# Optimization experiments

Hardware: AMD Instinct MI355X
Metric: run time of the kernel (lower is better)

Reference implementation:

```python
import jax, jax.numpy as jnp
import numpy as np

B, C, G, E, R, T, L, K = 8, 192, 256, 384, 4, 8192, 3, 3
DILATIONS = (1, 3, 9)
EPS = 1e-5


def setup_inputs() -> dict:
    key = jax.random.key(0)
    ks = jax.random.split(key, 16)
    s = 0.05
    return {
        'x': jax.random.normal(ks[0], (B, C, T), jnp.float32),
        'x_mask': jnp.ones((B, 1, T), jnp.float32),
        'g': jax.random.normal(ks[1], (B, G, 1), jnp.float32),
        'dconv_w': jax.random.normal(ks[2], (L, C, K), jnp.float32) * s,
        'dconv_b': jax.random.normal(ks[3], (L, C), jnp.float32) * s,
        'ln_gamma': jnp.ones((L, C), jnp.float32),
        'ln_beta': jnp.zeros((L, C), jnp.float32),
        'p1_w': jax.random.normal(ks[4], (L, E, C), jnp.float32) * s,
        'p1_b': jax.random.normal(ks[5], (L, E), jnp.float32) * s,
        'p1_ain_w': jax.random.normal(ks[6], (L, C * R, G), jnp.float32) * 0.01,
        'p1_ain_b': jnp.zeros((L, C * R), jnp.float32),
        'p1_aout_w': jax.random.normal(ks[7], (L, E * R, G), jnp.float32) * 0.01,
        'p1_aout_b': jnp.zeros((L, E * R), jnp.float32),
        'p2_w': jax.random.normal(ks[8], (L, C, E), jnp.float32) * s,
        'p2_b': jax.random.normal(ks[9], (L, C), jnp.float32) * s,
        'p2_ain_w': jax.random.normal(ks[10], (L, E * R, G), jnp.float32) * 0.01,
        'p2_ain_b': jnp.zeros((L, E * R), jnp.float32),
        'p2_aout_w': jax.random.normal(ks[11], (L, C * R, G), jnp.float32) * 0.01,
        'p2_aout_b': jnp.zeros((L, C * R), jnp.float32),
    }


def _causal_dconv(x, w, b, dilation):
    # x: [B,C,T]; w: [C,K] depthwise kernel; matches flip/pad/conv/flip in torch module
    xf = jnp.flip(x, 2)
    xf = jnp.pad(xf, ((0, 0), (0, 0), (0, (K - 1) * dilation)))
    y = jax.lax.conv_general_dilated(
        xf, w[:, None, :], window_strides=(1,), padding='VALID',
        rhs_dilation=(dilation,), dimension_numbers=('NCH', 'OIH', 'NCH'),
        feature_group_count=C)
    y = y + b[None, :, None]
    return jnp.flip(y, 2)


def _layernorm_c(x, gamma, beta):
    # LayerNorm over channel axis (axis=1)
    mu = jnp.mean(x, axis=1, keepdims=True)
    var = jnp.mean(jnp.square(x - mu), axis=1, keepdims=True)
    xn = (x - mu) * jax.lax.rsqrt(var + EPS)
    return xn * gamma[None, :, None] + beta[None, :, None]


def _lora(x, g2, w_main, b_main, ain_w, ain_b, aout_w, aout_b, cin, cout):
    # main 1x1 conv
    x_ = jnp.einsum('oc,bcl->bol', w_main, x) + b_main[None, :, None]
    a_in = (g2 @ ain_w.T + ain_b).reshape(-1, cin, R)      # [B,cin,R]
    a_out = (g2 @ aout_w.T + aout_b).reshape(-1, R, cout)  # [B,R,cout]
    t = jnp.einsum('bcl,bcr->brl', x, a_in)
    low = jnp.einsum('brl,brc->bcl', t, a_out)
    return x_ + low


def reference(x, x_mask, g, dconv_w, dconv_b, ln_gamma, ln_beta,
              p1_w, p1_b, p1_ain_w, p1_ain_b, p1_aout_w, p1_aout_b,
              p2_w, p2_b, p2_ain_w, p2_ain_b, p2_aout_w, p2_aout_b):
    g2 = g[:, :, 0]  # [B,G]
    x = x * x_mask
    for i in range(L):
        residual = x
        h = _causal_dconv(x, dconv_w[i], dconv_b[i], DILATIONS[i])
        h = _layernorm_c(h, ln_gamma[i], ln_beta[i])
        h = h * x_mask
        h = _lora(h, g2, p1_w[i], p1_b[i], p1_ain_w[i], p1_ain_b[i],
                  p1_aout_w[i], p1_aout_b[i], C, E)
        h = jax.nn.gelu(h, approximate=False)
        h = _lora(h, g2, p2_w[i], p2_b[i], p2_ain_w[i], p2_ain_b[i],
                  p2_aout_w[i], p2_aout_b[i], E, C)
        x = residual + h
    return x
```

## Files before the change

### kernel.cpp

```cpp
#include <hip/hip_runtime.h>
#include <hip/hip_bf16.h>

#define B_ 8
#define C_ 192
#define G_ 256
#define E_ 384
#define R_ 4
#define T_ 8192
#define L_ 3
#define K_ 3

typedef __attribute__((ext_vector_type(4))) float f32x4;
typedef __attribute__((ext_vector_type(8))) short bf16x8;
typedef __attribute__((ext_vector_type(4))) short bf16x4;

static __device__ __forceinline__ float bf2f(short u) {
    union { float f; unsigned int i; } z;
    z.i = ((unsigned int)(unsigned short)u) << 16;
    return z.f;
}

static __device__ __forceinline__ float gelu_fast(float x) {
    float x2 = x * x;
    float inner = fmaf(0.044715f * x, x2, x);
    float e = __expf(1.5957691216057308f * inner);
    float r = 1.0f / (e + 1.0f);
    float t = fmaf(-2.0f, r, 1.0f);
    float s = 0.5f * x;
    return fmaf(s, t, s);
}

__global__ __launch_bounds__(256) void adapters_kernel(
    const float* __restrict__ g2,
    const float* __restrict__ w0, const float* __restrict__ bi0, float* __restrict__ o0,
    const float* __restrict__ w1, const float* __restrict__ bi1, float* __restrict__ o1,
    const float* __restrict__ w2, const float* __restrict__ bi2, float* __restrict__ o2,
    const float* __restrict__ w3, const float* __restrict__ bi3, float* __restrict__ o3)
{
    const int N0 = L_ * B_ * (C_ * R_);
    const int N1 = L_ * B_ * (E_ * R_);
    int idx = blockIdx.x * 256 + threadIdx.x;
    const float* w; const float* bi; float* o; int rows; int li;
    if (idx < N0)                      { w=w0; bi=bi0; o=o0; rows=C_*R_; li=idx; }
    else if ((idx -= N0) < N1)         { w=w1; bi=bi1; o=o1; rows=E_*R_; li=idx; }
    else if ((idx -= N1) < N1)         { w=w2; bi=bi2; o=o2; rows=E_*R_; li=idx; }
    else if ((idx -= N1) < N0)         { w=w3; bi=bi3; o=o3; rows=C_*R_; li=idx; }
    else return;
    int bb = li & 7;
    int lr = li >> 3;
    const float4* wr = (const float4*)(w + (size_t)lr * G_);
    const float4* gb = (const float4*)(g2 + (size_t)bb * G_);
    float s = bi[lr];
#pragma unroll 8
    for (int g = 0; g < G_ / 4; ++g) {
        float4 a = gb[g], b = wr[g];
        s = fmaf(a.x, b.x, s); s = fmaf(a.y, b.y, s);
        s = fmaf(a.z, b.z, s); s = fmaf(a.w, b.w, s);
    }
    o[((size_t)(lr / rows) * B_ + bb) * rows + (lr % rows)] = s;
}

__global__ __launch_bounds__(256) void builds_kernel(
    const float* __restrict__ p1w, const float* __restrict__ p2w,
    const float* __restrict__ A1in, const float* __restrict__ A1out,
    const float* __restrict__ A2in, const float* __restrict__ A2out,
    __hip_bfloat16* __restrict__ W1, __hip_bfloat16* __restrict__ W2)
{
    const int W1B = (L_ * B_ * E_ * C_) / 256;
    int blk = blockIdx.x;
    if (blk < W1B) {
        int idx = blk * 256 + threadIdx.x;
        int c = idx % C_;
        int e = (idx / C_) % E_;
        int b = (idx / (C_ * E_)) % B_;
        int l = idx / (C_ * E_ * B_);
        float v = p1w[((size_t)l * E_ + e) * C_ + c];
        const float* ai = A1in + ((size_t)l * B_ + b) * (C_ * R_);
        const float* ao = A1out + ((size_t)l * B_ + b) * (R_ * E_);
#pragma unroll
        for (int r = 0; r < R_; ++r) v = fmaf(ai[c * R_ + r], ao[r * E_ + e], v);
        W1[idx] = __float2bfloat16(v);
    } else {
        int idx = (blk - W1B) * 256 + threadIdx.x;
        int e = idx % E_;
        int c = (idx / E_) % C_;
        int b = (idx / (C_ * E_)) % B_;
        int l = idx / (C_ * E_ * B_);
        float v = p2w[((size_t)l * C_ + c) * E_ + e];
        const float* ai = A2in + ((size_t)l * B_ + b) * (E_ * R_);
        const float* ao = A2out + ((size_t)l * B_ + b) * (R_ * C_);
#pragma unroll
        for (int r = 0; r < R_; ++r) v = fmaf(ai[e * R_ + r], ao[r * C_ + c], v);
        W2[idx] = __float2bfloat16(v);
    }
}

__global__ __launch_bounds__(256) void transpose_in_kernel(
    const float* __restrict__ x, const float* __restrict__ mask,
    __hip_bfloat16* __restrict__ xw)
{
    __shared__ float tile[64][65];
    int b = blockIdx.z, c0 = blockIdx.y * 64, t0 = blockIdx.x * 64;
#pragma unroll
    for (int it = 0; it < 4; ++it) {
        int i = it * 256 + threadIdx.x;
        int r = i >> 4, cq = i & 15;
        float4 xv = *(const float4*)(&x[((size_t)b * C_ + c0 + r) * T_ + t0 + cq * 4]);
        float4 mv = *(const float4*)(&mask[(size_t)b * T_ + t0 + cq * 4]);
        tile[r][cq * 4 + 0] = xv.x * mv.x;
        tile[r][cq * 4 + 1] = xv.y * mv.y;
        tile[r][cq * 4 + 2] = xv.z * mv.z;
        tile[r][cq * 4 + 3] = xv.w * mv.w;
    }
    __syncthreads();
#pragma unroll
    for (int it = 0; it < 4; ++it) {
        int i = it * 256 + threadIdx.x;
        int r = i >> 4, cq = i & 15;
        union { __hip_bfloat16 h[4]; int2 i2; } u;
#pragma unroll
        for (int j = 0; j < 4; ++j) u.h[j] = __float2bfloat16(tile[cq * 4 + j][r]);
        *(int2*)(&xw[((size_t)b * T_ + t0 + r) * C_ + c0 + cq * 4]) = u.i2;
    }
}

__global__ __launch_bounds__(256, 2) void ffn_fused_kernel(
    const __hip_bfloat16* __restrict__ xin, __hip_bfloat16* __restrict__ xout,
    const float* __restrict__ dw, const float* __restrict__ db,
    const float* __restrict__ gamma, const float* __restrict__ beta,
    const float* __restrict__ mask,
    const __hip_bfloat16* __restrict__ W1, const float* __restrict__ b1,
    const __hip_bfloat16* __restrict__ W2, const float* __restrict__ b2,
    int dil, float* __restrict__ outF)
{
    __shared__ __align__(16) char smem[75776];
    __hip_bfloat16 (*Hs)[C_ + 8]  = (__hip_bfloat16 (*)[C_ + 8])smem;
    __hip_bfloat16 (*H1s)[E_ + 8] = (__hip_bfloat16 (*)[E_ + 8])(smem + 25600);

    const int bid = blockIdx.x;
    const int b = bid & 7;
    const int t0 = (bid >> 3) * 64;
    const int tid = threadIdx.x;
    const int wv = tid >> 6, lane = tid & 63;
    const int llo = lane & 15, lhi = lane >> 4;
    const size_t xbase = (size_t)b * T_ * C_;

    {
        const int grp = tid >> 4, gl = tid & 15;
        const int cbase = gl * 12;
        float4 wf[9], dbf[3], gaf[3], bef[3];
#pragma unroll
        for (int q = 0; q < 9; ++q) wf[q] = *(const float4*)(dw + cbase * 3 + q * 4);
#pragma unroll
        for (int q = 0; q < 3; ++q) {
            dbf[q] = *(const float4*)(db + cbase + q * 4);
            gaf[q] = *(const float4*)(gamma + cbase + q * 4);
            bef[q] = *(const float4*)(beta + cbase + q * 4);
        }
#pragma unroll
        for (int rr = 0; rr < 4; ++rr) {
            int tl = grp * 4 + rr;
            int t = t0 + tl;
            float v[12];
#pragma unroll
            for (int j = 0; j < 12; ++j) v[j] = ((const float*)dbf)[j];
#pragma unroll
            for (int k3 = 0; k3 < 3; ++k3) {
                int tt = t - k3 * dil;
                if (tt >= 0) {
                    const __hip_bfloat16* rp = xin + xbase + (size_t)tt * C_ + cbase;
#pragma unroll
                    for (int q = 0; q < 3; ++q) {
                        bf16x4 xv = *(const bf16x4*)(rp + q * 4);
#pragma unroll
                        for (int jj = 0; jj < 4; ++jj) {
                            int j = q * 4 + jj;
                            v[j] = fmaf(((const float*)wf)[j * 3 + k3], bf2f(xv[jj]), v[j]);
                        }
                    }
                }
            }
            float s = 0.f, sq = 0.f;
#pragma unroll
            for (int j = 0; j < 12; ++j) { s += v[j]; sq = fmaf(v[j], v[j], sq); }
#pragma unroll
            for (int o = 1; o <= 8; o <<= 1) {
                s += __shfl_xor(s, o, 64);
                sq += __shfl_xor(sq, o, 64);
            }
            float mu = s * (1.f / C_);
            float var = fmaf(sq, 1.f / C_, -mu * mu);
            float rs = rsqrtf(var + 1e-5f);
            float m = mask[(size_t)b * T_ + t];
            union { __hip_bfloat16 h[12]; int2 i2[3]; } u;
#pragma unroll
            for (int j = 0; j < 12; ++j) {
                float xn = (v[j] - mu) * rs;
                u.h[j] = __float2bfloat16(
                    fmaf(xn, ((const float*)gaf)[j], ((const float*)bef)[j]) * m);
            }
#pragma unroll
            for (int q = 0; q < 3; ++q)
                *(int2*)(&Hs[tl][cbase + q * 4]) = u.i2[q];
        }
    }
    __syncthreads();

    const __hip_bfloat16* w1p = W1 + (size_t)b * E_ * C_
        + (size_t)(wv * 96 + llo) * C_ + lhi * 8;
    f32x4 acc1[6][4] = {};
#pragma unroll
    for (int kc = 0; kc < 6; ++kc) {
        bf16x8 bfr[4];
#pragma unroll
        for (int nf = 0; nf < 4; ++nf)
            bfr[nf] = *(const bf16x8*)(&Hs[nf * 16 + llo][kc * 32 + lhi * 8]);
#pragma unroll
        for (int mf = 0; mf < 6; ++mf) {
            bf16x8 af = *(const bf16x8*)(w1p + (size_t)mf * 16 * C_ + kc * 32);
#pragma unroll
            for (int nf = 0; nf < 4; ++nf)
                acc1[mf][nf] = __builtin_amdgcn_mfma_f32_16x16x32_bf16(
                    af, bfr[nf], acc1[mf][nf], 0, 0, 0);
        }
    }

#pragma unroll
    for (int mf = 0; mf < 6; ++mf) {
        int e0 = wv * 96 + mf * 16 + lhi * 4;
        float4 b1v = *(const float4*)(b1 + e0);
#pragma unroll
        for (int nf = 0; nf < 4; ++nf) {
            union { __hip_bfloat16 h[4]; int2 i2; } u;
#pragma unroll
            for (int j = 0; j < 4; ++j) {
                float xx = acc1[mf][nf][j] + ((const float*)&b1v)[j];
                u.h[j] = __float2bfloat16(gelu_fast(xx));
            }
            *(int2*)(&H1s[nf * 16 + llo][e0]) = u.i2;
        }
    }
    __syncthreads();

    int2 resid[3][4];
#pragma unroll
    for (int mf = 0; mf < 3; ++mf) {
        int c0 = wv * 48 + mf * 16 + lhi * 4;
#pragma unroll
        for (int nf = 0; nf < 4; ++nf) {
            int t = t0 + nf * 16 + llo;
            resid[mf][nf] = *(const int2*)(xin + xbase + (size_t)t * C_ + c0);
        }
    }

    const __hip_bfloat16* w2p = W2 + (size_t)b * C_ * E_
        + (size_t)(wv * 48 + llo) * E_ + lhi * 8;
    f32x4 acc2[3][4] = {};
#pragma unroll
    for (int kc = 0; kc < 12; ++kc) {
        bf16x8 bfr[4];
#pragma unroll
        for (int nf = 0; nf < 4; ++nf)
            bfr[nf] = *(const bf16x8*)(&H1s[nf * 16 + llo][kc * 32 + lhi * 8]);
#pragma unroll
        for (int mf = 0; mf < 3; ++mf) {
            bf16x8 af = *(const bf16x8*)(w2p + (size_t)mf * 16 * E_ + kc * 32);
#pragma unroll
            for (int nf = 0; nf < 4; ++nf)
                acc2[mf][nf] = __builtin_amdgcn_mfma_f32_16x16x32_bf16(
                    af, bfr[nf], acc2[mf][nf], 0, 0, 0);
        }
    }

    if (outF == nullptr) {
#pragma unroll
        for (int mf = 0; mf < 3; ++mf) {
            int c0 = wv * 48 + mf * 16 + lhi * 4;
            float4 b2v = *(const float4*)(b2 + c0);
#pragma unroll
            for (int nf = 0; nf < 4; ++nf) {
                int t = t0 + nf * 16 + llo;
                __hip_bfloat16* po = xout + xbase + (size_t)t * C_ + c0;
                union { __hip_bfloat16 h[4]; int2 i2; } ui, uo;
                ui.i2 = resid[mf][nf];
#pragma unroll
                for (int j = 0; j < 4; ++j)
                    uo.h[j] = __float2bfloat16(
                        bf2f(*(short*)&ui.h[j]) + acc2[mf][nf][j] + ((const float*)&b2v)[j]);
                *(int2*)po = uo.i2;
            }
        }
    } else {
        float (*Tile)[68] = (float (*)[68])smem;
        __syncthreads();
#pragma unroll
        for (int mf = 0; mf < 3; ++mf) {
            int c0 = wv * 48 + mf * 16 + lhi * 4;
            float4 b2v = *(const float4*)(b2 + c0);
#pragma unroll
            for (int nf = 0; nf < 4; ++nf) {
                int tl = nf * 16 + llo;
                union { __hip_bfloat16 h[4]; int2 i2; } ui;
                ui.i2 = resid[mf][nf];
#pragma unroll
                for (int j = 0; j < 4; ++j)
                    Tile[c0 + j][tl] =
                        bf2f(*(short*)&ui.h[j]) + acc2[mf][nf][j] + ((const float*)&b2v)[j];
            }
        }
        __syncthreads();
#pragma unroll
        for (int it = 0; it < 12; ++it) {
            int i = it * 256 + tid;
            int r = i >> 4, tq = i & 15;
            float4 o = *(const float4*)(&Tile[r][tq * 4]);
            *(float4*)(&outF[((size_t)b * C_ + r) * T_ + t0 + tq * 4]) = o;
        }
    }
}

extern "C" void kernel_launch(void* const* d_in, const int* in_sizes, int n_in,
                              void* d_out, int out_size, void* d_ws, size_t ws_size,
                              hipStream_t stream) {
    const float* x        = (const float*)d_in[0];
    const float* x_mask   = (const float*)d_in[1];
    const float* g        = (const float*)d_in[2];
    const float* dconv_w  = (const float*)d_in[3];
    const float* dconv_b  = (const float*)d_in[4];
    const float* ln_gamma = (const float*)d_in[5];
    const float* ln_beta  = (const float*)d_in[6];
    const float* p1_w     = (const float*)d_in[7];
    const float* p1_b     = (const float*)d_in[8];
    const float* p1_ain_w = (const float*)d_in[9];
    const float* p1_ain_b = (const float*)d_in[10];
    const float* p1_aout_w= (const float*)d_in[11];
    const float* p1_aout_b= (const float*)d_in[12];
    const float* p2_w     = (const float*)d_in[13];
    const float* p2_b     = (const float*)d_in[14];
    const float* p2_ain_w = (const float*)d_in[15];
    const float* p2_ain_b = (const float*)d_in[16];
    const float* p2_aout_w= (const float*)d_in[17];
    const float* p2_aout_b= (const float*)d_in[18];

    char* ws = (char*)d_ws;
    size_t off = 0;
    __hip_bfloat16* xwA = (__hip_bfloat16*)(ws + off); off += (size_t)B_ * T_ * C_ * 2;
    __hip_bfloat16* xwB = (__hip_bfloat16*)(ws + off); off += (size_t)B_ * T_ * C_ * 2;
    __hip_bfloat16* W1 = (__hip_bfloat16*)(ws + off);  off += (size_t)L_ * B_ * E_ * C_ * 2;
    __hip_bfloat16* W2 = (__hip_bfloat16*)(ws + off);  off += (size_t)L_ * B_ * C_ * E_ * 2;
    float* A1in  = (float*)(ws + off); off += (size_t)L_ * B_ * C_ * R_ * 4;
    float* A1out = (float*)(ws + off); off += (size_t)L_ * B_ * R_ * E_ * 4;
    float* A2in  = (float*)(ws + off); off += (size_t)L_ * B_ * E_ * R_ * 4;
    float* A2out = (float*)(ws + off); off += (size_t)L_ * B_ * R_ * C_ * 4;

    {
        int total = L_ * B_ * (2 * C_ * R_ + 2 * E_ * R_);
        adapters_kernel<<<(total + 255) / 256, 256, 0, stream>>>(
            g,
            p1_ain_w, p1_ain_b, A1in,
            p1_aout_w, p1_aout_b, A1out,
            p2_ain_w, p2_ain_b, A2in,
            p2_aout_w, p2_aout_b, A2out);
    }
    {
        int w1blocks = (L_ * B_ * E_ * C_) / 256;
        builds_kernel<<<2 * w1blocks, 256, 0, stream>>>(
            p1_w, p2_w, A1in, A1out, A2in, A2out, W1, W2);
    }

    transpose_in_kernel<<<dim3(T_ / 64, C_ / 64, B_), 256, 0, stream>>>(x, x_mask, xwA);

    const int DILS[3] = {1, 3, 9};
    __hip_bfloat16* bufs[2] = {xwA, xwB};
    for (int l = 0; l < L_; ++l) {
        float* outF = (l == L_ - 1) ? (float*)d_out : nullptr;
        ffn_fused_kernel<<<(T_ / 64) * B_, 256, 0, stream>>>(
            bufs[l & 1], bufs[(l & 1) ^ 1],
            dconv_w + l * C_ * K_, dconv_b + l * C_,
            ln_gamma + l * C_, ln_beta + l * C_, x_mask,
            W1 + (size_t)l * B_ * E_ * C_, p1_b + l * E_,
            W2 + (size_t)l * B_ * C_ * E_, p2_b + l * C_, DILS[l], outF);
    }
}
```

Baseline: 232.3 us.

## Process two time tiles per block and prefetch next tile's conv inputs

The fused FFN kernel is templated on tiles per block, and the first two layers now run two 64-step tiles per block with half the grid. The next tile's dilated-conv inputs are loaded into registers before the current tile's GEMMs, so global latency overlaps with MFMA work. Residual loads move to the epilogue. The cost is many more live registers (36 bf16x4 staging values) under launch_bounds(256,2), which risks spills or lower occupancy, and the smaller grid gives less parallelism.

```diff
diff --git a/kernel.cpp b/kernel.cpp
--- a/kernel.cpp
+++ b/kernel.cpp
@@ -124,6 +124,91 @@
     }
 }
 
+struct StageRegs { bf16x4 xv[4][3][3]; };
+
+static __device__ __forceinline__ void stage_load(
+    const __hip_bfloat16* __restrict__ xin, size_t xbase,
+    int t0s, int dil, int grp, int cbase, StageRegs& sr)
+{
+#pragma unroll
+    for (int rr = 0; rr < 4; ++rr) {
+        int t = t0s + grp * 4 + rr;
+#pragma unroll
+        for (int k3 = 0; k3 < 3; ++k3) {
+            int tt = t - k3 * dil;
+            bool ok = (tt >= 0);
+            const __hip_bfloat16* rp =
+                xin + xbase + (size_t)(ok ? tt : 0) * C_ + cbase;
+#pragma unroll
+            for (int q = 0; q < 3; ++q) {
+                bf16x4 z = *(const bf16x4*)(rp + q * 4);
+                if (!ok) z = (bf16x4){0, 0, 0, 0};
+                sr.xv[rr][k3][q] = z;
+            }
+        }
+    }
+}
+
+static __device__ __forceinline__ void stage_compute(
+    const StageRegs& sr,
+    const float* __restrict__ dw, const float* __restrict__ db,
+    const float* __restrict__ gamma, const float* __restrict__ beta,
+    const float* __restrict__ mask,
+    int b, int t0s, int grp, int cbase,
+    __hip_bfloat16 (* __restrict__ Hst)[C_ + 8])
+{
+    float4 wf[9], dbf[3], gaf[3], bef[3];
+#pragma unroll
+    for (int q = 0; q < 9; ++q) wf[q] = *(const float4*)(dw + cbase * 3 + q * 4);
+#pragma unroll
+    for (int q = 0; q < 3; ++q) {
+        dbf[q] = *(const float4*)(db + cbase + q * 4);
+        gaf[q] = *(const float4*)(gamma + cbase + q * 4);
+        bef[q] = *(const float4*)(beta + cbase + q * 4);
+    }
+#pragma unroll
+    for (int rr = 0; rr < 4; ++rr) {
+        int tl = grp * 4 + rr;
+        int t = t0s + tl;
+        float v[12];
+#pragma unroll
+        for (int j = 0; j < 12; ++j) v[j] = ((const float*)dbf)[j];
+#pragma unroll
+        for (int k3 = 0; k3 < 3; ++k3)
+#pragma unroll
+            for (int q = 0; q < 3; ++q)
+#pragma unroll
+                for (int jj = 0; jj < 4; ++jj) {
+                    int j = q * 4 + jj;
+                    v[j] = fmaf(((const float*)wf)[j * 3 + k3],
+                                bf2f(sr.xv[rr][k3][q][jj]), v[j]);
+                }
+        float s = 0.f, sq = 0.f;
+#pragma unroll
+        for (int j = 0; j < 12; ++j) { s += v[j]; sq = fmaf(v[j], v[j], sq); }
+#pragma unroll
+        for (int o = 1; o <= 8; o <<= 1) {
+            s += __shfl_xor(s, o, 64);
+            sq += __shfl_xor(sq, o, 64);
+        }
+        float mu = s * (1.f / C_);
+        float var = fmaf(sq, 1.f / C_, -mu * mu);
+        float rs = rsqrtf(var + 1e-5f);
+        float m = mask[(size_t)b * T_ + t];
+        union { __hip_bfloat16 h[12]; int2 i2[3]; } u;
+#pragma unroll
+        for (int j = 0; j < 12; ++j) {
+            float xn = (v[j] - mu) * rs;
+            u.h[j] = __float2bfloat16(
+                fmaf(xn, ((const float*)gaf)[j], ((const float*)bef)[j]) * m);
+        }
+#pragma unroll
+        for (int q = 0; q < 3; ++q)
+            *(int2*)(&Hst[tl][cbase + q * 4]) = u.i2[q];
+    }
+}
+
+template<int NT, bool LAST>
 __global__ __launch_bounds__(256, 2) void ffn_fused_kernel(
     const __hip_bfloat16* __restrict__ xin, __hip_bfloat16* __restrict__ xout,
     const float* __restrict__ dw, const float* __restrict__ db,
@@ -139,182 +224,130 @@
 
     const int bid = blockIdx.x;
     const int b = bid & 7;
-    const int t0 = (bid >> 3) * 64;
+    const int tbase = (bid >> 3) * 64 * NT;
     const int tid = threadIdx.x;
     const int wv = tid >> 6, lane = tid & 63;
     const int llo = lane & 15, lhi = lane >> 4;
+    const int grp = tid >> 4, cbase = (tid & 15) * 12;
     const size_t xbase = (size_t)b * T_ * C_;
-
-    {
-        const int grp = tid >> 4, gl = tid & 15;
-        const int cbase = gl * 12;
-        float4 wf[9], dbf[3], gaf[3], bef[3];
-#pragma unroll
-        for (int q = 0; q < 9; ++q) wf[q] = *(const float4*)(dw + cbase * 3 + q * 4);
-#pragma unroll
-        for (int q = 0; q < 3; ++q) {
-            dbf[q] = *(const float4*)(db + cbase + q * 4);
-            gaf[q] = *(const float4*)(gamma + cbase + q * 4);
-            bef[q] = *(const float4*)(beta + cbase + q * 4);
-        }
-#pragma unroll
-        for (int rr = 0; rr < 4; ++rr) {
-            int tl = grp * 4 + rr;
-            int t = t0 + tl;
-            float v[12];
-#pragma unroll
-            for (int j = 0; j < 12; ++j) v[j] = ((const float*)dbf)[j];
-#pragma unroll
-            for (int k3 = 0; k3 < 3; ++k3) {
-                int tt = t - k3 * dil;
-                if (tt >= 0) {
-                    const __hip_bfloat16* rp = xin + xbase + (size_t)tt * C_ + cbase;
-#pragma unroll
-                    for (int q = 0; q < 3; ++q) {
-                        bf16x4 xv = *(const bf16x4*)(rp + q * 4);
-#pragma unroll
-                        for (int jj = 0; jj < 4; ++jj) {
-                            int j = q * 4 + jj;
-                            v[j] = fmaf(((const float*)wf)[j * 3 + k3], bf2f(xv[jj]), v[j]);
-                        }
-                    }
+    const __hip_bfloat16* W1b = W1 + (size_t)b * E_ * C_;
+    const __hip_bfloat16* W2b = W2 + (size_t)b * C_ * E_;
+
+    StageRegs sr;
+    stage_load(xin, xbase, tbase, dil, grp, cbase, sr);
+    stage_compute(sr, dw, db, gamma, beta, mask, b, tbase, grp, cbase, Hs);
+    __syncthreads();
+
+#pragma unroll
+    for (int it = 0; it < NT; ++it) {
+        const int t0 = tbase + it * 64;
+
+        if (it + 1 < NT)
+            stage_load(xin, xbase, t0 + 64, dil, grp, cbase, sr);
+
+        const __hip_bfloat16* w1p = W1b + (size_t)(wv * 96 + llo) * C_ + lhi * 8;
+        f32x4 acc1[6][4] = {};
+#pragma unroll
+        for (int kc = 0; kc < 6; ++kc) {
+            bf16x8 bfr[4];
+#pragma unroll
+            for (int nf = 0; nf < 4; ++nf)
+                bfr[nf] = *(const bf16x8*)(&Hs[nf * 16 + llo][kc * 32 + lhi * 8]);
+#pragma unroll
+            for (int mf = 0; mf < 6; ++mf) {
+                bf16x8 af = *(const bf16x8*)(w1p + (size_t)mf * 16 * C_ + kc * 32);
+#pragma unroll
+                for (int nf = 0; nf < 4; ++nf)
+                    acc1[mf][nf] = __builtin_amdgcn_mfma_f32_16x16x32_bf16(
+                        af, bfr[nf], acc1[mf][nf], 0, 0, 0);
+            }
+        }
+
+#pragma unroll
+        for (int mf = 0; mf < 6; ++mf) {
+            int e0 = wv * 96 + mf * 16 + lhi * 4;
+            float4 b1v = *(const float4*)(b1 + e0);
+#pragma unroll
+            for (int nf = 0; nf < 4; ++nf) {
+                union { __hip_bfloat16 h[4]; int2 i2; } u;
+#pragma unroll
+                for (int j = 0; j < 4; ++j) {
+                    float xx = acc1[mf][nf][j] + ((const float*)&b1v)[j];
+                    u.h[j] = __float2bfloat16(gelu_fast(xx));
                 }
-            }
-            float s = 0.f, sq = 0.f;
-#pragma unroll
-            for (int j = 0; j < 12; ++j) { s += v[j]; sq = fmaf(v[j], v[j], sq); }
-#pragma unroll
-            for (int o = 1; o <= 8; o <<= 1) {
-                s += __shfl_xor(s, o, 64);
-                sq += __shfl_xor(sq, o, 64);
-            }
-            float mu = s * (1.f / C_);
-            float var = fmaf(sq, 1.f / C_, -mu * mu);
-            float rs = rsqrtf(var + 1e-5f);
-            float m = mask[(size_t)b * T_ + t];
-            union { __hip_bfloat16 h[12]; int2 i2[3]; } u;
-#pragma unroll
-            for (int j = 0; j < 12; ++j) {
-                float xn = (v[j] - mu) * rs;
-                u.h[j] = __float2bfloat16(
-                    fmaf(xn, ((const float*)gaf)[j], ((const float*)bef)[j]) * m);
-            }
-#pragma unroll
-            for (int q = 0; q < 3; ++q)
-                *(int2*)(&Hs[tl][cbase + q * 4]) = u.i2[q];
-        }
-    }
-    __syncthreads();
-
-    const __hip_bfloat16* w1p = W1 + (size_t)b * E_ * C_
-        + (size_t)(wv * 96 + llo) * C_ + lhi * 8;
-    f32x4 acc1[6][4] = {};
-#pragma unroll
-    for (int kc = 0; kc < 6; ++kc) {
-        bf16x8 bfr[4];
-#pragma unroll
-        for (int nf = 0; nf < 4; ++nf)
-            bfr[nf] = *(const bf16x8*)(&Hs[nf * 16 + llo][kc * 32 + lhi * 8]);
-#pragma unroll
-        for (int mf = 0; mf < 6; ++mf) {
-            bf16x8 af = *(const bf16x8*)(w1p + (size_t)mf * 16 * C_ + kc * 32);
+                *(int2*)(&H1s[nf * 16 + llo][e0]) = u.i2;
+            }
+        }
+        __syncthreads();
+
+        const __hip_bfloat16* w2p = W2b + (size_t)(wv * 48 + llo) * E_ + lhi * 8;
+        f32x4 acc2[3][4] = {};
+#pragma unroll
+        for (int kc = 0; kc < 12; ++kc) {
+            bf16x8 bfr[4];
 #pragma unroll
             for (int nf = 0; nf < 4; ++nf)
-                acc1[mf][nf] = __builtin_amdgcn_mfma_f32_16x16x32_bf16(
-                    af, bfr[nf], acc1[mf][nf], 0, 0, 0);
-        }
-    }
-
-#pragma unroll
-    for (int mf = 0; mf < 6; ++mf) {
-        int e0 = wv * 96 + mf * 16 + lhi * 4;
-        float4 b1v = *(const float4*)(b1 + e0);
-#pragma unroll
-        for (int nf = 0; nf < 4; ++nf) {
-            union { __hip_bfloat16 h[4]; int2 i2; } u;
-#pragma unroll
-            for (int j = 0; j < 4; ++j) {
-                float xx = acc1[mf][nf][j] + ((const float*)&b1v)[j];
-                u.h[j] = __float2bfloat16(gelu_fast(xx));
-            }
-            *(int2*)(&H1s[nf * 16 + llo][e0]) = u.i2;
-        }
-    }
-    __syncthreads();
-
-    int2 resid[3][4];
-#pragma unroll
-    for (int mf = 0; mf < 3; ++mf) {
-        int c0 = wv * 48 + mf * 16 + lhi * 4;
-#pragma unroll
-        for (int nf = 0; nf < 4; ++nf) {
-            int t = t0 + nf * 16 + llo;
-            resid[mf][nf] = *(const int2*)(xin + xbase + (size_t)t * C_ + c0);
-        }
-    }
-
-    const __hip_bfloat16* w2p = W2 + (size_t)b * C_ * E_
-        + (size_t)(wv * 48 + llo) * E_ + lhi * 8;
-    f32x4 acc2[3][4] = {};
-#pragma unroll
-    for (int kc = 0; kc < 12; ++kc) {
-        bf16x8 bfr[4];
-#pragma unroll
-        for (int nf = 0; nf < 4; ++nf)
-            bfr[nf] = *(const bf16x8*)(&H1s[nf * 16 + llo][kc * 32 + lhi * 8]);
-#pragma unroll
-        for (int mf = 0; mf < 3; ++mf) {
-            bf16x8 af = *(const bf16x8*)(w2p + (size_t)mf * 16 * E_ + kc * 32);
-#pragma unroll
-            for (int nf = 0; nf < 4; ++nf)
-                acc2[mf][nf] = __builtin_amdgcn_mfma_f32_16x16x32_bf16(
-                    af, bfr[nf], acc2[mf][nf], 0, 0, 0);
-        }
-    }
-
-    if (outF == nullptr) {
-#pragma unroll
-        for (int mf = 0; mf < 3; ++mf) {
-            int c0 = wv * 48 + mf * 16 + lhi * 4;
-            float4 b2v = *(const float4*)(b2 + c0);
-#pragma unroll
-            for (int nf = 0; nf < 4; ++nf) {
-                int t = t0 + nf * 16 + llo;
-                __hip_bfloat16* po = xout + xbase + (size_t)t * C_ + c0;
-                union { __hip_bfloat16 h[4]; int2 i2; } ui, uo;
-                ui.i2 = resid[mf][nf];
-#pragma unroll
-                for (int j = 0; j < 4; ++j)
-                    uo.h[j] = __float2bfloat16(
-                        bf2f(*(short*)&ui.h[j]) + acc2[mf][nf][j] + ((const float*)&b2v)[j]);
-                *(int2*)po = uo.i2;
-            }
-        }
-    } else {
-        float (*Tile)[68] = (float (*)[68])smem;
-        __syncthreads();
-#pragma unroll
-        for (int mf = 0; mf < 3; ++mf) {
-            int c0 = wv * 48 + mf * 16 + lhi * 4;
-            float4 b2v = *(const float4*)(b2 + c0);
-#pragma unroll
-            for (int nf = 0; nf < 4; ++nf) {
-                int tl = nf * 16 + llo;
-                union { __hip_bfloat16 h[4]; int2 i2; } ui;
-                ui.i2 = resid[mf][nf];
-#pragma unroll
-                for (int j = 0; j < 4; ++j)
-                    Tile[c0 + j][tl] =
-                        bf2f(*(short*)&ui.h[j]) + acc2[mf][nf][j] + ((const float*)&b2v)[j];
-            }
-        }
-        __syncthreads();
-#pragma unroll
-        for (int it = 0; it < 12; ++it) {
-            int i = it * 256 + tid;
-            int r = i >> 4, tq = i & 15;
-            float4 o = *(const float4*)(&Tile[r][tq * 4]);
-            *(float4*)(&outF[((size_t)b * C_ + r) * T_ + t0 + tq * 4]) = o;
+                bfr[nf] = *(const bf16x8*)(&H1s[nf * 16 + llo][kc * 32 + lhi * 8]);
+#pragma unroll
+            for (int mf = 0; mf < 3; ++mf) {
+                bf16x8 af = *(const bf16x8*)(w2p + (size_t)mf * 16 * E_ + kc * 32);
+#pragma unroll
+                for (int nf = 0; nf < 4; ++nf)
+                    acc2[mf][nf] = __builtin_amdgcn_mfma_f32_16x16x32_bf16(
+                        af, bfr[nf], acc2[mf][nf], 0, 0, 0);
+            }
+        }
+
+        if (!LAST) {
+#pragma unroll
+            for (int mf = 0; mf < 3; ++mf) {
+                int c0 = wv * 48 + mf * 16 + lhi * 4;
+                float4 b2v = *(const float4*)(b2 + c0);
+#pragma unroll
+                for (int nf = 0; nf < 4; ++nf) {
+                    int t = t0 + nf * 16 + llo;
+                    const __hip_bfloat16* pr = xin + xbase + (size_t)t * C_ + c0;
+                    __hip_bfloat16* po = xout + xbase + (size_t)t * C_ + c0;
+                    union { __hip_bfloat16 h[4]; int2 i2; } ui, uo;
+                    ui.i2 = *(const int2*)pr;
+#pragma unroll
+                    for (int j = 0; j < 4; ++j)
+                        uo.h[j] = __float2bfloat16(
+                            bf2f(*(short*)&ui.h[j]) + acc2[mf][nf][j] + ((const float*)&b2v)[j]);
+                    *(int2*)po = uo.i2;
+                }
+            }
+            if (it + 1 < NT) {
+                stage_compute(sr, dw, db, gamma, beta, mask, b, t0 + 64, grp, cbase, Hs);
+                __syncthreads();
+            }
+        } else {
+            float (*Tile)[68] = (float (*)[68])smem;
+            __syncthreads();
+#pragma unroll
+            for (int mf = 0; mf < 3; ++mf) {
+                int c0 = wv * 48 + mf * 16 + lhi * 4;
+                float4 b2v = *(const float4*)(b2 + c0);
+#pragma unroll
+                for (int nf = 0; nf < 4; ++nf) {
+                    int tl = nf * 16 + llo;
+                    const __hip_bfloat16* pr = xin + xbase + (size_t)(t0 + tl) * C_ + c0;
+                    union { __hip_bfloat16 h[4]; int2 i2; } ui;
+                    ui.i2 = *(const int2*)pr;
+#pragma unroll
+                    for (int j = 0; j < 4; ++j)
+                        Tile[c0 + j][tl] =
+                            bf2f(*(short*)&ui.h[j]) + acc2[mf][nf][j] + ((const float*)&b2v)[j];
+                }
+            }
+            __syncthreads();
+#pragma unroll
+            for (int it2 = 0; it2 < 12; ++it2) {
+                int i = it2 * 256 + tid;
+                int r = i >> 4, tq = i & 15;
+                float4 o = *(const float4*)(&Tile[r][tq * 4]);
+                *(float4*)(&outF[((size_t)b * C_ + r) * T_ + t0 + tq * 4]) = o;
+            }
         }
     }
 }
@@ -373,12 +406,20 @@
     const int DILS[3] = {1, 3, 9};
     __hip_bfloat16* bufs[2] = {xwA, xwB};
     for (int l = 0; l < L_; ++l) {
-        float* outF = (l == L_ - 1) ? (float*)d_out : nullptr;
-        ffn_fused_kernel<<<(T_ / 64) * B_, 256, 0, stream>>>(
-            bufs[l & 1], bufs[(l & 1) ^ 1],
-            dconv_w + l * C_ * K_, dconv_b + l * C_,
-            ln_gamma + l * C_, ln_beta + l * C_, x_mask,
-            W1 + (size_t)l * B_ * E_ * C_, p1_b + l * E_,
-            W2 + (size_t)l * B_ * C_ * E_, p2_b + l * C_, DILS[l], outF);
-    }
-}
+        if (l < L_ - 1) {
+            ffn_fused_kernel<2, false><<<(T_ / 128) * B_, 256, 0, stream>>>(
+                bufs[l & 1], bufs[(l & 1) ^ 1],
+                dconv_w + l * C_ * K_, dconv_b + l * C_,
+                ln_gamma + l * C_, ln_beta + l * C_, x_mask,
+                W1 + (size_t)l * B_ * E_ * C_, p1_b + l * E_,
+                W2 + (size_t)l * B_ * C_ * E_, p2_b + l * C_, DILS[l], nullptr);
+        } else {
+            ffn_fused_kernel<1, true><<<(T_ / 64) * B_, 256, 0, stream>>>(
+                bufs[l & 1], bufs[(l & 1) ^ 1],
+                dconv_w + l * C_ * K_, dconv_b + l * C_,
+                ln_gamma + l * C_, ln_beta + l * C_, x_mask,
+                W1 + (size_t)l * B_ * E_ * C_, p1_b + l * E_,
+                W2 + (size_t)l * B_ * C_ * E_, p2_b + l * C_, DILS[l], (float*)d_out);
+        }
+    }
+}
```

Result: no change. 228.0 us, median of 5 (-1.9%).
